# Performance work log

Hardware: AMD Instinct MI355X
Metric: run time of the kernel (lower is better)

## Reference

```python
import jax, jax.numpy as jnp
import numpy as np

N_NODES = 50000
N_EDGES = 800000
ND = 64
ED = 32
MSG = 128
HID = 256
N_AGENTS = 25000


def setup_inputs() -> dict:
    key = jax.random.key(0)
    ks = jax.random.split(key, 12)
    s = lambda k, shape, fan: jax.random.normal(k, shape, jnp.float32) / np.sqrt(fan)
    return {
        'node_feats': jax.random.normal(ks[0], (N_NODES, ND), jnp.float32),
        'edge_feats': jax.random.normal(ks[1], (N_EDGES, ED), jnp.float32),
        'W_msg1': s(ks[2], (2 * ND + ED, HID), 2 * ND + ED),
        'b_msg1': jnp.zeros((HID,), jnp.float32),
        'W_msg2': s(ks[3], (HID, MSG), HID),
        'b_msg2': jnp.zeros((MSG,), jnp.float32),
        'w_gate': s(ks[4], (MSG, 1), MSG),
        'b_gate': jnp.zeros((1,), jnp.float32),
        'W_h1': s(ks[5], (MSG, HID), MSG),
        'b_h1': jnp.zeros((HID,), jnp.float32),
        'W_h2': s(ks[6], (HID, HID), HID),
        'b_h2': jnp.zeros((HID,), jnp.float32),
        'W_out': s(ks[7], (HID, 1), HID),
        'b_out': jnp.zeros((1,), jnp.float32),
        'senders': jax.random.randint(ks[8], (N_EDGES,), 0, N_NODES, jnp.int32),
        'receivers': jax.random.randint(ks[9], (N_EDGES,), 0, N_NODES, jnp.int32),
        'n_agents': N_AGENTS,
    }


def reference(node_feats, edge_feats, W_msg1, b_msg1, W_msg2, b_msg2,
              w_gate, b_gate, W_h1, b_h1, W_h2, b_h2, W_out, b_out,
              senders, receivers, n_agents):
    n_nodes = node_feats.shape[0]
    # gather sender/receiver features, build edge messages (gather-transform)
    msg_in = jnp.concatenate(
        [node_feats[senders], node_feats[receivers], edge_feats], axis=-1)  # [E, 2*ND+ED]
    h = jax.nn.relu(msg_in @ W_msg1 + b_msg1)                               # [E, HID]
    msg = jax.nn.relu(h @ W_msg2 + b_msg2)                                  # [E, MSG]
    # per-receiver segment softmax attention
    logits = (msg @ w_gate + b_gate)[:, 0]                                  # [E]
    seg_max = jax.ops.segment_max(logits, receivers, num_segments=n_nodes)  # [N]
    e = jnp.exp(logits - seg_max[receivers])                                # [E]
    denom = jax.ops.segment_sum(e, receivers, num_segments=n_nodes)         # [N]
    attn = e / (denom[receivers] + 1e-9)                                    # [E]
    # scatter-aggregate messages to nodes
    aggr = jax.ops.segment_sum(attn[:, None] * msg, receivers,
                               num_segments=n_nodes)                        # [N, MSG]
    # node_type == 0: agent nodes are the first n_agents nodes
    x = aggr[:n_agents]                                                     # [A, MSG]
    # head MLP
    x = jax.nn.relu(x @ W_h1 + b_h1)
    x = jax.nn.relu(x @ W_h2 + b_h2)
    # Dense(1) + tanh
    return jnp.tanh(x @ W_out + b_out)                                      # [A, 1]
```

## Files before the change

kernel.cpp:

```cpp
#include <hip/hip_runtime.h>
#include <hip/hip_bf16.h>

#define N_NODES  50000
#define N_EDGES  800000
#define ND       64
#define ED       32
#define MSGD     128
#define HIDD     256
#define N_AGENTS 25000
#define EPAD     800064

typedef _Float16 f16;
typedef __attribute__((ext_vector_type(4))) _Float16 f16x4;
typedef __attribute__((ext_vector_type(8))) _Float16 f16x8;
typedef __attribute__((ext_vector_type(4))) float f32x4;
typedef unsigned short u16;
typedef unsigned int   u32;
typedef unsigned long long u64;

__global__ __launch_bounds__(256) void compact_pack_kernel(
    const int* __restrict__ recv, const float* __restrict__ nf,
    f16* __restrict__ nf16, int* __restrict__ rankb, int* __restrict__ deg,
    const float* __restrict__ W1, const float* __restrict__ W2,
    const float* __restrict__ Wh1, const float* __restrict__ Wh2,
    f16* __restrict__ F1, f16* __restrict__ F2,
    f16* __restrict__ F3, f16* __restrict__ F4)
{
    int b = blockIdx.x;
    if (b >= N_EDGES / 256) {
        int tid  = (b - N_EDGES / 256) * 256 + threadIdx.x;
        int grp  = tid >> 6, lane = tid & 63;
        const float* W; f16* D; int NT, stride, gl;
        if      (grp < 80)  { W = W1;  D = F1; NT = 16; stride = 256; gl = grp; }
        else if (grp < 144) { W = W2;  D = F2; NT = 8;  stride = 128; gl = grp - 80; }
        else if (grp < 208) { W = Wh1; D = F3; NT = 16; stride = 256; gl = grp - 144; }
        else if (grp < 336) { W = Wh2; D = F4; NT = 16; stride = 256; gl = grp - 208; }
        else return;
        int ks = gl / NT, nt = gl - ks * NT;
        int n  = nt * 16 + (lane & 15);
        int k0 = ks * 32 + (lane >> 4) * 8;
        f16* dst = D + ((size_t)gl * 64 + lane) * 8;
        #pragma unroll
        for (int j = 0; j < 8; ++j)
            dst[j] = (f16)W[(size_t)(k0 + j) * stride + n];
        return;
    }
    int i = b * 256 + threadIdx.x;
    {
        float4 v = ((const float4*)nf)[i];
        f16x4 h;
        h.x = (f16)v.x; h.y = (f16)v.y; h.z = (f16)v.z; h.w = (f16)v.w;
        ((f16x4*)nf16)[i] = h;
    }
    int r = recv[i];
    if (r < N_AGENTS)
        rankb[i] = atomicAdd(&deg[r], 1);
}

__global__ __launch_bounds__(1024) void prefix_part(
    const int* __restrict__ deg, int* __restrict__ bsum)
{
    __shared__ int red[16];
    int b = blockIdx.x, t = threadIdx.x;
    int v = (t < 1000) ? deg[b * 1000 + t] : 0;
    #pragma unroll
    for (int k = 1; k <= 32; k <<= 1) v += __shfl_xor(v, k, 64);
    if ((t & 63) == 0) red[t >> 6] = v;
    __syncthreads();
    if (t == 0) {
        int s = 0;
        #pragma unroll
        for (int w = 0; w < 16; ++w) s += red[w];
        bsum[b] = s;
    }
}

__global__ __launch_bounds__(1024) void prefix_scan(
    const int* __restrict__ deg, const int* __restrict__ bsum,
    int* __restrict__ off)
{
    __shared__ int part[1024];
    __shared__ int basesh;
    int b = blockIdx.x, t = threadIdx.x;
    if (t == 0) {
        int s = 0;
        for (int j = 0; j < b; ++j) s += bsum[j];
        basesh = s;
    }
    int v = (t < 1000) ? deg[b * 1000 + t] : 0;
    part[t] = v;
    __syncthreads();
    for (int d = 1; d < 1024; d <<= 1) {
        int u = (t >= d) ? part[t - d] : 0;
        __syncthreads();
        part[t] += u;
        __syncthreads();
    }
    int incl = part[t];
    int base = basesh;
    if (t < 1000) off[b * 1000 + t] = base + incl - v;
    if (b == 24 && t == 999) off[N_AGENTS] = base + incl;
}

__global__ __launch_bounds__(256) void scatter_kernel(
    const int* __restrict__ recv, const int* __restrict__ send,
    const int* __restrict__ rankb, const int* __restrict__ off,
    int4* __restrict__ idx4)
{
    int i = blockIdx.x * 256 + threadIdx.x;
    int r = recv[i];
    if (r < N_AGENTS) {
        int pos = off[r] + rankb[i];
        idx4[pos] = make_int4(i, send[i], r, 0);
    }
}

__global__ __launch_bounds__(512, 4) void edge_mlp_mfma(
    const f16* __restrict__ nf16, const float* __restrict__ ef,
    const f16* __restrict__ F1, const f16* __restrict__ F2,
    const float* __restrict__ b1, const float* __restrict__ b2,
    const float* __restrict__ wg, const float* __restrict__ bg,
    const int* __restrict__ idx4i, const int* __restrict__ cnt,
    f16* __restrict__ msg_out, float* __restrict__ evals)
{
    __shared__ __align__(16) f16 XF[2][10][64][8];
    __shared__ __align__(16) f16 HB[16][64][8];
    __shared__ __align__(16) f16 msgt[32][136];
    __shared__ float lpart[8][32];

    const int tid  = threadIdx.x;
    const int wv   = tid >> 6;
    const int lane = tid & 63;
    const int q    = lane >> 4;
    const int li   = lane & 15;
    const int cntv   = cnt[0];
    const int ntiles = (cntv + 31) >> 5;

    const int xcd   = blockIdx.x & 7;
    const int bslot = blockIdx.x >> 3;
    const int tstep = gridDim.x >> 3;
    const int T8    = (ntiles + 7) >> 3;
    const int tend  = min((xcd + 1) * T8, ntiles);
    const int t0    = xcd * T8 + bslot;

    f16x8 w1[2][5], w2[8];
    #pragma unroll
    for (int ntl = 0; ntl < 2; ++ntl)
        #pragma unroll
        for (int ks = 0; ks < 5; ++ks)
            w1[ntl][ks] = *(const f16x8*)(F1 + (((size_t)(ks * 16 + 2 * wv + ntl)) * 64 + lane) * 8);
    #pragma unroll
    for (int ks = 0; ks < 8; ++ks)
        w2[ks] = *(const f16x8*)(F2 + (((size_t)(ks * 8 + wv)) * 64 + lane) * 8);

    const float4 ba  = *(const float4*)&b1[wv * 32 + q * 4];
    const float4 bb  = *(const float4*)&b1[wv * 32 + 16 + q * 4];
    const float4 bc  = *(const float4*)&b2[wv * 16 + q * 4];
    const float4 wg4 = *(const float4*)&wg[wv * 16 + q * 4];
    const float  bgv = bg[0];

    if (t0 < tend) {
        const int e0p = t0 * 32;
        f16 (*XFd)[64][8] = XF[0];
        for (int idx = tid; idx < 768; idx += 512) {
            int e = idx / 24, g = idx - e * 24;
            int cp = e0p + e;
            if (g < 16) {
                int node = idx4i[cp * 4 + ((g < 8) ? 1 : 2)];
                f16x8 h = *(const f16x8*)(nf16 + (size_t)node * 64 + (g & 7) * 8);
                int slt = (e >> 4) * 5 + (g >> 2);
                int ln  = (e & 15) + 16 * (g & 3);
                *(f16x8*)&XFd[slt][ln][0] = h;
            } else {
                int eid = idx4i[cp * 4];
                float4 v = ((const float4*)ef)[(size_t)eid * 8 + (g - 16)];
                int k0  = 128 + (g - 16) * 4;
                int slt = (e >> 4) * 5 + 4;
                int ln  = (e & 15) + 16 * ((k0 & 31) >> 3);
                int j0  = k0 & 7;
                f16x4 h;
                h.x = (f16)v.x; h.y = (f16)v.y; h.z = (f16)v.z; h.w = (f16)v.w;
                *(f16x4*)&XFd[slt][ln][j0] = h;
            }
        }
    }
    __syncthreads();

    int p = 0;
    for (int t = t0; t < tend; t += tstep) {
        const int e0 = t * 32;
        const int tn = t + tstep;

        if (tn < tend) {
            const int e0n = tn * 32;
            f16 (*XFd)[64][8] = XF[p ^ 1];
            for (int idx = tid; idx < 768; idx += 512) {
                int e = idx / 24, g = idx - e * 24;
                int cp = e0n + e;
                if (g < 16) {
                    int node = idx4i[cp * 4 + ((g < 8) ? 1 : 2)];
                    f16x8 h = *(const f16x8*)(nf16 + (size_t)node * 64 + (g & 7) * 8);
                    int slt = (e >> 4) * 5 + (g >> 2);
                    int ln  = (e & 15) + 16 * (g & 3);
                    *(f16x8*)&XFd[slt][ln][0] = h;
                } else {
                    int eid = idx4i[cp * 4];
                    float4 v = ((const float4*)ef)[(size_t)eid * 8 + (g - 16)];
                    int k0  = 128 + (g - 16) * 4;
                    int slt = (e >> 4) * 5 + 4;
                    int ln  = (e & 15) + 16 * ((k0 & 31) >> 3);
                    int j0  = k0 & 7;
                    f16x4 h;
                    h.x = (f16)v.x; h.y = (f16)v.y; h.z = (f16)v.z; h.w = (f16)v.w;
                    *(f16x4*)&XFd[slt][ln][j0] = h;
                }
            }
        }

        f32x4 acc[2][2];
        acc[0][0] = f32x4{ba.x, ba.y, ba.z, ba.w}; acc[1][0] = acc[0][0];
        acc[0][1] = f32x4{bb.x, bb.y, bb.z, bb.w}; acc[1][1] = acc[0][1];
        #pragma unroll
        for (int ks = 0; ks < 5; ++ks)
            #pragma unroll
            for (int eh = 0; eh < 2; ++eh) {
                f16x8 xh = *(const f16x8*)XF[p][eh * 5 + ks][lane];
                acc[eh][0] = __builtin_amdgcn_mfma_f32_16x16x32_f16(w1[0][ks], xh, acc[eh][0], 0, 0, 0);
                acc[eh][1] = __builtin_amdgcn_mfma_f32_16x16x32_f16(w1[1][ks], xh, acc[eh][1], 0, 0, 0);
            }
        #pragma unroll
        for (int eh = 0; eh < 2; ++eh)
            #pragma unroll
            for (int ntl = 0; ntl < 2; ++ntl) {
                f16x4 hv;
                hv.x = (f16)fmaxf(acc[eh][ntl][0], 0.f);
                hv.y = (f16)fmaxf(acc[eh][ntl][1], 0.f);
                hv.z = (f16)fmaxf(acc[eh][ntl][2], 0.f);
                hv.w = (f16)fmaxf(acc[eh][ntl][3], 0.f);
                int l2 = li + 16 * (2 * ntl + (q >> 1));
                int j0 = (q & 1) * 4;
                *(f16x4*)&HB[eh * 8 + wv][l2][j0] = hv;
            }
        __syncthreads();

        f32x4 acc2[2];
        acc2[0] = f32x4{bc.x, bc.y, bc.z, bc.w}; acc2[1] = acc2[0];
        #pragma unroll
        for (int ks2 = 0; ks2 < 8; ++ks2)
            #pragma unroll
            for (int eh = 0; eh < 2; ++eh) {
                f16x8 hh = *(const f16x8*)HB[eh * 8 + ks2][lane];
                acc2[eh] = __builtin_amdgcn_mfma_f32_16x16x32_f16(w2[ks2], hh, acc2[eh], 0, 0, 0);
            }
        {
            float pr[2];
            #pragma unroll
            for (int eh = 0; eh < 2; ++eh) {
                float v0 = fmaxf(acc2[eh][0], 0.f);
                float v1 = fmaxf(acc2[eh][1], 0.f);
                float v2 = fmaxf(acc2[eh][2], 0.f);
                float v3 = fmaxf(acc2[eh][3], 0.f);
                f16x4 mm;
                mm.x = (f16)v0; mm.y = (f16)v1; mm.z = (f16)v2; mm.w = (f16)v3;
                *(f16x4*)&msgt[eh * 16 + li][wv * 16 + q * 4] = mm;
                float pp = v0 * wg4.x + v1 * wg4.y + v2 * wg4.z + v3 * wg4.w;
                pp += __shfl_xor(pp, 16, 64);
                pp += __shfl_xor(pp, 32, 64);
                pr[eh] = pp;
            }
            if (lane < 16) {
                lpart[wv][li]      = pr[0];
                lpart[wv][16 + li] = pr[1];
            }
        }
        __syncthreads();

        {
            int row = tid >> 4, cg = tid & 15;
            *(uint4*)(msg_out + (size_t)(e0 + row) * 128 + cg * 8) =
                *(const uint4*)&msgt[row][cg * 8];
        }
        if (tid < 32) {
            float s2 = bgv;
            #pragma unroll
            for (int w = 0; w < 8; ++w) s2 += lpart[w][tid];
            evals[e0 + tid] = expf(s2);
        }
        p ^= 1;
    }
}

__global__ __launch_bounds__(1024, 4) void agg_agent_mfma(
    const int* __restrict__ off, const float* __restrict__ evals,
    const f16* __restrict__ msg,
    const f16* __restrict__ F3, const f16* __restrict__ F4,
    const float* __restrict__ bh1, const float* __restrict__ bh2,
    const float* __restrict__ Wout, const float* __restrict__ bout,
    float* __restrict__ out)
{
    __shared__ __align__(16) f16 XA[8][64][8];
    __shared__ __align__(16) f16 HB2[16][64][8];
    __shared__ float lpart[16][32];

    const int tid  = threadIdx.x;
    const int wv   = tid >> 6;
    const int lane = tid & 63;
    const int q    = lane >> 4;
    const int li   = lane & 15;
    const int a0i  = blockIdx.x * 32;

    {
        int g = tid >> 5, c = tid & 31;
        int r = a0i + g;
        float den = 1e-9f;
        float4 acc = make_float4(0.f, 0.f, 0.f, 0.f);
        if (r < N_AGENTS) {
            int beg = off[r], end = off[r + 1];
            const u64* mp = (const u64*)(msg + (size_t)beg * 128) + c;
            int pp = beg;
            for (; pp + 3 < end; pp += 4, mp += 128) {
                float e0 = evals[pp], e1 = evals[pp + 1];
                float e2 = evals[pp + 2], e3 = evals[pp + 3];
                u64 u0 = mp[0], u1 = mp[32], u2 = mp[64], u3 = mp[96];
                den += (e0 + e1) + (e2 + e3);
                union { u64 u; f16 h[4]; } c0, c1, c2, c3;
                c0.u = u0; c1.u = u1; c2.u = u2; c3.u = u3;
                acc.x = fmaf(e3, (float)c3.h[0], fmaf(e2, (float)c2.h[0],
                        fmaf(e1, (float)c1.h[0], fmaf(e0, (float)c0.h[0], acc.x))));
                acc.y = fmaf(e3, (float)c3.h[1], fmaf(e2, (float)c2.h[1],
                        fmaf(e1, (float)c1.h[1], fmaf(e0, (float)c0.h[1], acc.y))));
                acc.z = fmaf(e3, (float)c3.h[2], fmaf(e2, (float)c2.h[2],
                        fmaf(e1, (float)c1.h[2], fmaf(e0, (float)c0.h[2], acc.z))));
                acc.w = fmaf(e3, (float)c3.h[3], fmaf(e2, (float)c2.h[3],
                        fmaf(e1, (float)c1.h[3], fmaf(e0, (float)c0.h[3], acc.w))));
            }
            for (; pp < end; ++pp, mp += 32) {
                float e = evals[pp];
                den += e;
                union { u64 u; f16 h[4]; } cv; cv.u = *mp;
                acc.x = fmaf(e, (float)cv.h[0], acc.x);
                acc.y = fmaf(e, (float)cv.h[1], acc.y);
                acc.z = fmaf(e, (float)cv.h[2], acc.z);
                acc.w = fmaf(e, (float)cv.h[3], acc.w);
            }
        }
        float inv = 1.0f / den;
        int k0   = c * 4;
        int slot = (g >> 4) * 4 + (k0 >> 5);
        int ln   = (g & 15) + 16 * ((k0 & 31) >> 3);
        int j0   = k0 & 7;
        f16x4 h;
        h.x = (f16)(acc.x * inv); h.y = (f16)(acc.y * inv);
        h.z = (f16)(acc.z * inv); h.w = (f16)(acc.w * inv);
        *(f16x4*)&XA[slot][ln][j0] = h;
    }
    __syncthreads();

    f16x8 wh1[4], wh2[8];
    #pragma unroll
    for (int ks = 0; ks < 4; ++ks)
        wh1[ks] = *(const f16x8*)(F3 + (((size_t)(ks * 16 + wv)) * 64 + lane) * 8);
    #pragma unroll
    for (int ks = 0; ks < 8; ++ks)
        wh2[ks] = *(const f16x8*)(F4 + (((size_t)(ks * 16 + wv)) * 64 + lane) * 8);

    f32x4 acc[2] = {};
    #pragma unroll
    for (int ks = 0; ks < 4; ++ks)
        #pragma unroll
        for (int eh = 0; eh < 2; ++eh) {
            f16x8 xh = *(const f16x8*)XA[eh * 4 + ks][lane];
            acc[eh] = __builtin_amdgcn_mfma_f32_16x16x32_f16(wh1[ks], xh, acc[eh], 0, 0, 0);
        }
    {
        const float4 b1v = ((const float4*)bh1)[wv * 4 + q];
        #pragma unroll
        for (int eh = 0; eh < 2; ++eh) {
            f16x4 hv;
            hv.x = (f16)fmaxf(acc[eh][0] + b1v.x, 0.f);
            hv.y = (f16)fmaxf(acc[eh][1] + b1v.y, 0.f);
            hv.z = (f16)fmaxf(acc[eh][2] + b1v.z, 0.f);
            hv.w = (f16)fmaxf(acc[eh][3] + b1v.w, 0.f);
            int l2 = li + 16 * ((wv & 1) * 2 + (q >> 1));
            int j0 = (q & 1) * 4;
            *(f16x4*)&HB2[eh * 8 + (wv >> 1)][l2][j0] = hv;
        }
    }
    __syncthreads();

    f32x4 acc2[2] = {};
    #pragma unroll
    for (int ks2 = 0; ks2 < 8; ++ks2)
        #pragma unroll
        for (int eh = 0; eh < 2; ++eh) {
            f16x8 hh = *(const f16x8*)HB2[eh * 8 + ks2][lane];
            acc2[eh] = __builtin_amdgcn_mfma_f32_16x16x32_f16(wh2[ks2], hh, acc2[eh], 0, 0, 0);
        }
    {
        const float4 b2v = ((const float4*)bh2)[wv * 4 + q];
        const float4 wo4 = ((const float4*)Wout)[wv * 4 + q];
        float pr[2];
        #pragma unroll
        for (int eh = 0; eh < 2; ++eh) {
            float pp = fmaxf(acc2[eh][0] + b2v.x, 0.f) * wo4.x
                     + fmaxf(acc2[eh][1] + b2v.y, 0.f) * wo4.y
                     + fmaxf(acc2[eh][2] + b2v.z, 0.f) * wo4.z
                     + fmaxf(acc2[eh][3] + b2v.w, 0.f) * wo4.w;
            pp += __shfl_xor(pp, 16, 64);
            pp += __shfl_xor(pp, 32, 64);
            pr[eh] = pp;
        }
        if (lane < 16) {
            lpart[wv][li]      = pr[0];
            lpart[wv][16 + li] = pr[1];
        }
    }
    __syncthreads();

    if (tid < 32 && a0i + tid < N_AGENTS) {
        float s = bout[0];
        #pragma unroll
        for (int w = 0; w < 16; ++w) s += lpart[w][tid];
        out[a0i + tid] = tanhf(s);
    }
}

extern "C" void kernel_launch(void* const* d_in, const int* in_sizes, int n_in,
                              void* d_out, int out_size, void* d_ws, size_t ws_size,
                              hipStream_t stream)
{
    const float* nf   = (const float*)d_in[0];
    const float* ef   = (const float*)d_in[1];
    const float* W1   = (const float*)d_in[2];
    const float* b1   = (const float*)d_in[3];
    const float* W2   = (const float*)d_in[4];
    const float* b2   = (const float*)d_in[5];
    const float* wg   = (const float*)d_in[6];
    const float* bg   = (const float*)d_in[7];
    const float* Wh1  = (const float*)d_in[8];
    const float* bh1  = (const float*)d_in[9];
    const float* Wh2  = (const float*)d_in[10];
    const float* bh2  = (const float*)d_in[11];
    const float* Wout = (const float*)d_in[12];
    const float* bout = (const float*)d_in[13];
    const int*   send = (const int*)d_in[14];
    const int*   recv = (const int*)d_in[15];

    char* ws = (char*)d_ws;
    int*  deg   = (int*)ws;            ws += (size_t)N_AGENTS * 4;
    int4* idx4  = (int4*)ws;           ws += (size_t)EPAD * 16;
    size_t zero_bytes = (size_t)(ws - (char*)d_ws);
    int* rankb  = (int*)ws;            ws += (size_t)N_EDGES * 4;
    int* bsum   = (int*)ws;            ws += 32 * 4;
    int* off    = (int*)ws;            ws += (size_t)(N_AGENTS + 8) * 4;
    float* evals = (float*)ws;         ws += (size_t)EPAD * 4;
    f16* nf16   = (f16*)ws;            ws += (size_t)N_NODES * ND * 2;
    f16* F1     = (f16*)ws;            ws += (size_t)160 * 256 * 2;
    f16* F2     = (f16*)ws;            ws += (size_t)256 * 128 * 2;
    f16* F3     = (f16*)ws;            ws += (size_t)128 * 256 * 2;
    f16* F4     = (f16*)ws;            ws += (size_t)256 * 256 * 2;
    f16* msg    = (f16*)ws;

    hipMemsetAsync(d_ws, 0, zero_bytes, stream);

    compact_pack_kernel<<<N_EDGES / 256 + 84, 256, 0, stream>>>(
        recv, nf, nf16, rankb, deg, W1, W2, Wh1, Wh2, F1, F2, F3, F4);
    prefix_part<<<25, 1024, 0, stream>>>(deg, bsum);
    prefix_scan<<<25, 1024, 0, stream>>>(deg, bsum, off);
    scatter_kernel<<<N_EDGES / 256, 256, 0, stream>>>(
        recv, send, rankb, off, idx4);
    edge_mlp_mfma<<<512, 512, 0, stream>>>(
        nf16, ef, F1, F2, b1, b2, wg, bg, (const int*)idx4, off + N_AGENTS,
        msg, evals);
    agg_agent_mfma<<<(N_AGENTS + 31) / 32, 1024, 0, stream>>>(
        off, evals, msg, F3, F4, bh1, bh2, Wout, bout, (float*)d_out);
}
```

Before: 364.6 us.

## Pre-permute edge features to fp16 in scatter; XCD-aware agent block mapping

The scatter kernel now converts each kept edge's features to fp16 and writes them in sorted receiver order. The edge MLP can then load them contiguously with 16-byte loads instead of gathering fp32 rows by edge id. The aggregation kernel remaps block indices so that contiguous agent ranges sit on the same XCD, which may improve L2 locality for the sorted message reads. The cost is extra workspace and a strided fp32 read plus fp16 write in the scatter pass, and a fallback path is kept for when the workspace is too small.

```diff
diff --git a/kernel.cpp b/kernel.cpp
--- a/kernel.cpp
+++ b/kernel.cpp
@@ -105,18 +105,30 @@
 __global__ __launch_bounds__(256) void scatter_kernel(
     const int* __restrict__ recv, const int* __restrict__ send,
     const int* __restrict__ rankb, const int* __restrict__ off,
-    int4* __restrict__ idx4)
+    int4* __restrict__ idx4, const float* __restrict__ ef,
+    f16* __restrict__ efc)
 {
     int i = blockIdx.x * 256 + threadIdx.x;
     int r = recv[i];
     if (r < N_AGENTS) {
         int pos = off[r] + rankb[i];
         idx4[pos] = make_int4(i, send[i], r, 0);
+        if (efc) {
+            f16* dst = efc + (size_t)pos * 32;
+            #pragma unroll
+            for (int k = 0; k < 8; ++k) {
+                float4 v = ((const float4*)ef)[(size_t)i * 8 + k];
+                f16x4 h;
+                h.x = (f16)v.x; h.y = (f16)v.y; h.z = (f16)v.z; h.w = (f16)v.w;
+                *(f16x4*)(dst + k * 4) = h;
+            }
+        }
     }
 }
 
 __global__ __launch_bounds__(512, 4) void edge_mlp_mfma(
     const f16* __restrict__ nf16, const float* __restrict__ ef,
+    const f16* __restrict__ efc,
     const f16* __restrict__ F1, const f16* __restrict__ F2,
     const float* __restrict__ b1, const float* __restrict__ b2,
     const float* __restrict__ wg, const float* __restrict__ bg,
@@ -142,6 +154,7 @@
     const int T8    = (ntiles + 7) >> 3;
     const int tend  = min((xcd + 1) * T8, ntiles);
     const int t0    = xcd * T8 + bslot;
+    const bool use_efc = (efc != nullptr);
 
     f16x8 w1[2][5], w2[8];
     #pragma unroll
@@ -162,41 +175,28 @@
     if (t0 < tend) {
         const int e0p = t0 * 32;
         f16 (*XFd)[64][8] = XF[0];
-        for (int idx = tid; idx < 768; idx += 512) {
-            int e = idx / 24, g = idx - e * 24;
-            int cp = e0p + e;
-            if (g < 16) {
-                int node = idx4i[cp * 4 + ((g < 8) ? 1 : 2)];
-                f16x8 h = *(const f16x8*)(nf16 + (size_t)node * 64 + (g & 7) * 8);
-                int slt = (e >> 4) * 5 + (g >> 2);
-                int ln  = (e & 15) + 16 * (g & 3);
-                *(f16x8*)&XFd[slt][ln][0] = h;
-            } else {
-                int eid = idx4i[cp * 4];
-                float4 v = ((const float4*)ef)[(size_t)eid * 8 + (g - 16)];
-                int k0  = 128 + (g - 16) * 4;
-                int slt = (e >> 4) * 5 + 4;
-                int ln  = (e & 15) + 16 * ((k0 & 31) >> 3);
-                int j0  = k0 & 7;
-                f16x4 h;
-                h.x = (f16)v.x; h.y = (f16)v.y; h.z = (f16)v.z; h.w = (f16)v.w;
-                *(f16x4*)&XFd[slt][ln][j0] = h;
-            }
-        }
-    }
-    __syncthreads();
-
-    int p = 0;
-    for (int t = t0; t < tend; t += tstep) {
-        const int e0 = t * 32;
-        const int tn = t + tstep;
-
-        if (tn < tend) {
-            const int e0n = tn * 32;
-            f16 (*XFd)[64][8] = XF[p ^ 1];
+        if (use_efc) {
+            for (int idx = tid; idx < 640; idx += 512) {
+                int e = idx / 20, g = idx - e * 20;
+                int cp = e0p + e;
+                if (g < 16) {
+                    int node = idx4i[cp * 4 + ((g < 8) ? 1 : 2)];
+                    f16x8 h = *(const f16x8*)(nf16 + (size_t)node * 64 + (g & 7) * 8);
+                    int slt = (e >> 4) * 5 + (g >> 2);
+                    int ln  = (e & 15) + 16 * (g & 3);
+                    *(f16x8*)&XFd[slt][ln][0] = h;
+                } else {
+                    f16x8 h = *(const f16x8*)(efc + (size_t)cp * 32 + (g - 16) * 8);
+                    int k0  = 128 + (g - 16) * 8;
+                    int slt = (e >> 4) * 5 + 4;
+                    int ln  = (e & 15) + 16 * ((k0 & 31) >> 3);
+                    *(f16x8*)&XFd[slt][ln][0] = h;
+                }
+            }
+        } else {
             for (int idx = tid; idx < 768; idx += 512) {
                 int e = idx / 24, g = idx - e * 24;
-                int cp = e0n + e;
+                int cp = e0p + e;
                 if (g < 16) {
                     int node = idx4i[cp * 4 + ((g < 8) ? 1 : 2)];
                     f16x8 h = *(const f16x8*)(nf16 + (size_t)node * 64 + (g & 7) * 8);
@@ -216,6 +216,59 @@
                 }
             }
         }
+    }
+    __syncthreads();
+
+    int p = 0;
+    for (int t = t0; t < tend; t += tstep) {
+        const int e0 = t * 32;
+        const int tn = t + tstep;
+
+        if (tn < tend) {
+            const int e0n = tn * 32;
+            f16 (*XFd)[64][8] = XF[p ^ 1];
+            if (use_efc) {
+                for (int idx = tid; idx < 640; idx += 512) {
+                    int e = idx / 20, g = idx - e * 20;
+                    int cp = e0n + e;
+                    if (g < 16) {
+                        int node = idx4i[cp * 4 + ((g < 8) ? 1 : 2)];
+                        f16x8 h = *(const f16x8*)(nf16 + (size_t)node * 64 + (g & 7) * 8);
+                        int slt = (e >> 4) * 5 + (g >> 2);
+                        int ln  = (e & 15) + 16 * (g & 3);
+                        *(f16x8*)&XFd[slt][ln][0] = h;
+                    } else {
+                        f16x8 h = *(const f16x8*)(efc + (size_t)cp * 32 + (g - 16) * 8);
+                        int k0  = 128 + (g - 16) * 8;
+                        int slt = (e >> 4) * 5 + 4;
+                        int ln  = (e & 15) + 16 * ((k0 & 31) >> 3);
+                        *(f16x8*)&XFd[slt][ln][0] = h;
+                    }
+                }
+            } else {
+                for (int idx = tid; idx < 768; idx += 512) {
+                    int e = idx / 24, g = idx - e * 24;
+                    int cp = e0n + e;
+                    if (g < 16) {
+                        int node = idx4i[cp * 4 + ((g < 8) ? 1 : 2)];
+                        f16x8 h = *(const f16x8*)(nf16 + (size_t)node * 64 + (g & 7) * 8);
+                        int slt = (e >> 4) * 5 + (g >> 2);
+                        int ln  = (e & 15) + 16 * (g & 3);
+                        *(f16x8*)&XFd[slt][ln][0] = h;
+                    } else {
+                        int eid = idx4i[cp * 4];
+                        float4 v = ((const float4*)ef)[(size_t)eid * 8 + (g - 16)];
+                        int k0  = 128 + (g - 16) * 4;
+                        int slt = (e >> 4) * 5 + 4;
+                        int ln  = (e & 15) + 16 * ((k0 & 31) >> 3);
+                        int j0  = k0 & 7;
+                        f16x4 h;
+                        h.x = (f16)v.x; h.y = (f16)v.y; h.z = (f16)v.z; h.w = (f16)v.w;
+                        *(f16x4*)&XFd[slt][ln][j0] = h;
+                    }
+                }
+            }
+        }
 
         f32x4 acc[2][2];
         acc[0][0] = f32x4{ba.x, ba.y, ba.z, ba.w}; acc[1][0] = acc[0][0];
@@ -307,7 +360,11 @@
     const int lane = tid & 63;
     const int q    = lane >> 4;
     const int li   = lane & 15;
-    const int a0i  = blockIdx.x * 32;
+    const int xcd   = blockIdx.x & 7;
+    const int bslot = blockIdx.x >> 3;
+    const int bidx  = xcd * 98 + bslot;
+    if (bidx * 32 >= N_AGENTS) return;
+    const int a0i  = bidx * 32;
 
     {
         int g = tid >> 5, c = tid & 31;
@@ -459,7 +516,10 @@
     f16* F2     = (f16*)ws;            ws += (size_t)256 * 128 * 2;
     f16* F3     = (f16*)ws;            ws += (size_t)128 * 256 * 2;
     f16* F4     = (f16*)ws;            ws += (size_t)256 * 256 * 2;
-    f16* msg    = (f16*)ws;
+    f16* msg    = (f16*)ws;            ws += (size_t)EPAD * 128 * 2;
+    f16* efc    = (f16*)ws;            ws += (size_t)EPAD * 32 * 2;
+    size_t needed = (size_t)(ws - (char*)d_ws);
+    if (needed > ws_size) efc = nullptr;
 
     hipMemsetAsync(d_ws, 0, zero_bytes, stream);
 
@@ -468,10 +528,10 @@
     prefix_part<<<25, 1024, 0, stream>>>(deg, bsum);
     prefix_scan<<<25, 1024, 0, stream>>>(deg, bsum, off);
     scatter_kernel<<<N_EDGES / 256, 256, 0, stream>>>(
-        recv, send, rankb, off, idx4);
+        recv, send, rankb, off, idx4, ef, efc);
     edge_mlp_mfma<<<512, 512, 0, stream>>>(
-        nf16, ef, F1, F2, b1, b2, wg, bg, (const int*)idx4, off + N_AGENTS,
-        msg, evals);
-    agg_agent_mfma<<<(N_AGENTS + 31) / 32, 1024, 0, stream>>>(
+        nf16, ef, efc, F1, F2, b1, b2, wg, bg, (const int*)idx4,
+        off + N_AGENTS, msg, evals);
+    agg_agent_mfma<<<784, 1024, 0, stream>>>(
         off, evals, msg, F3, F4, bh1, bh2, Wout, bout, (float*)d_out);
 }
```

After: 352.9 us. 3.2% less time.
